# Performance work log

Measured on AMD Instinct MI355X. Metric: run time of the kernel, lower is better.

## Reference

```python
import jax, jax.numpy as jnp
import numpy as np

B, S, D = 4, 512, 256
VOCAB, MAX_RULES = 50257, 1024
EPS = 1e-12  # F.normalize default eps


def setup_inputs() -> dict:
    key = jax.random.key(0)
    k1, k2, k3, k4 = jax.random.split(key, 4)
    hidden_states = jax.random.normal(k1, (B, S, D), dtype=jnp.float32)
    token_ids = jax.random.randint(k2, (B, S), 0, VOCAB, dtype=jnp.int64)
    rule_transform = jax.random.normal(k3, (MAX_RULES, D, D), dtype=jnp.float32)
    token_rules = jax.random.randint(k4, (VOCAB,), 0, MAX_RULES, dtype=jnp.int64)
    return {
        "hidden_states": hidden_states,
        "token_ids": token_ids,
        "rule_transform": rule_transform,
        "token_rules": token_rules,
    }


def reference(hidden_states, token_ids, rule_transform, token_rules):
    # per-token rule index: [B, S]
    rule_indices = token_rules[token_ids]
    # gather DxD rule matrix per token: [B, S, D, D]
    rule_matrices = rule_transform[rule_indices]
    # F.normalize(p=2, dim=(-2,-1)): divide by Frobenius norm per matrix
    fro = jnp.sqrt(jnp.sum(rule_matrices * rule_matrices, axis=(-2, -1), keepdims=True))
    rule_matrices = rule_matrices / jnp.maximum(fro, EPS)
    # batched matvec: [B,S,D] x [B,S,D,E] -> [B,S,E]
    return jnp.einsum("bsd,bsde->bse", hidden_states, rule_matrices)
```

## Files before the change

### kernel.cpp

```cpp
#include <hip/hip_runtime.h>
#include <math.h>

#define D 256
#define NRULES 1024
#define TPB 4
#define NTOK_MAX 4096

__global__ __launch_bounds__(1024) void prep_kernel(
    const int* __restrict__ token_ids,
    const int* __restrict__ token_rules,
    int ntok,
    int* __restrict__ starts,
    int* __restrict__ bucket,
    int* __restrict__ worklist,
    int* __restrict__ nwork)
{
    __shared__ int cnt[NRULES];
    __shared__ int rtok[NTOK_MAX];
    __shared__ int wl[NRULES];
    __shared__ int nw;

    const int t = threadIdx.x;
    cnt[t] = 0;
    if (t == 0) nw = 0;
    __syncthreads();

    for (int i = t; i < ntok; i += 1024) {
        const int r = token_rules[token_ids[i]];
        rtok[i] = r;
        atomicAdd(&cnt[r], 1);
    }
    __syncthreads();

    const int c = cnt[t];

    #pragma unroll
    for (int off = 1; off < NRULES; off <<= 1) {
        const int add = (t >= off) ? cnt[t - off] : 0;
        __syncthreads();
        cnt[t] += add;
        __syncthreads();
    }
    const int incl = cnt[t];
    const int excl = incl - c;
    starts[t] = excl;
    if (t == NRULES - 1) starts[NRULES] = incl;

    if (c > TPB) wl[atomicAdd(&nw, 1)] = t;
    __syncthreads();
    if (c > 0 && c <= TPB) wl[atomicAdd(&nw, 1)] = t;

    __syncthreads();
    cnt[t] = excl;
    __syncthreads();

    for (int i = t; i < ntok; i += 1024) {
        const int pos = atomicAdd(&cnt[rtok[i]], 1);
        bucket[pos] = i;
    }

    const int nwv = nw;
    for (int i = t; i < nwv; i += 1024) worklist[i] = wl[i];
    if (t == 0) nwork[0] = nwv;
}

__global__ __launch_bounds__(256) void process_kernel(
    const float* __restrict__ hidden,
    const float* __restrict__ rules,
    const int*   __restrict__ starts,
    const int*   __restrict__ bucket,
    const int*   __restrict__ worklist,
    const int*   __restrict__ nwork,
    float* __restrict__ out)
{
    if ((int)blockIdx.x >= nwork[0]) return;
    const int r     = worklist[blockIdx.x];
    const int start = starts[r];
    const int count = starts[r + 1] - start;

    const int t    = threadIdx.x;
    const int wave = t >> 6;
    const int lane = t & 63;

    __shared__ float h_lds[TPB][D];
    __shared__ float y_lds[TPB][4][D];
    __shared__ float sq_lds[4];
    __shared__ int   toks[TPB];

    const float* __restrict__ M = rules + (size_t)r * D * D;
    const int d0  = wave << 6;
    const int col = lane << 2;

    for (int base = 0; base < count; base += TPB) {
        if (t < TPB)
            toks[t] = (base + t < count) ? bucket[start + base + t] : -1;
        #pragma unroll
        for (int j = 0; j < TPB; ++j) {
            const int idx = base + j;
            h_lds[j][t] = (idx < count)
                ? hidden[(size_t)bucket[start + idx] * D + t] : 0.f;
        }
        __syncthreads();

        float4 acc[TPB];
        #pragma unroll
        for (int j = 0; j < TPB; ++j) acc[j] = float4{0.f, 0.f, 0.f, 0.f};
        float sq = 0.f;

        #pragma unroll 4
        for (int i = 0; i < 64; ++i) {
            const int d = d0 + i;
            const float4 m = *reinterpret_cast<const float4*>(M + (size_t)d * D + col);
            sq = fmaf(m.x, m.x, fmaf(m.y, m.y, fmaf(m.z, m.z, fmaf(m.w, m.w, sq))));
            #pragma unroll
            for (int j = 0; j < TPB; ++j) {
                const float h = h_lds[j][d];
                acc[j].x = fmaf(h, m.x, acc[j].x);
                acc[j].y = fmaf(h, m.y, acc[j].y);
                acc[j].z = fmaf(h, m.z, acc[j].z);
                acc[j].w = fmaf(h, m.w, acc[j].w);
            }
        }

        #pragma unroll
        for (int off = 32; off > 0; off >>= 1)
            sq += __shfl_down(sq, off, 64);
        if (lane == 0) sq_lds[wave] = sq;

        #pragma unroll
        for (int j = 0; j < TPB; ++j)
            *reinterpret_cast<float4*>(&y_lds[j][wave][col]) = acc[j];
        __syncthreads();

        const float fro2 = sq_lds[0] + sq_lds[1] + sq_lds[2] + sq_lds[3];
        const float inv  = 1.0f / fmaxf(sqrtf(fro2), 1e-12f);

        #pragma unroll
        for (int j = 0; j < TPB; ++j) {
            const int tok = toks[j];
            if (tok >= 0) {
                const float v = (y_lds[j][0][t] + y_lds[j][1][t] +
                                 y_lds[j][2][t] + y_lds[j][3][t]) * inv;
                out[(size_t)tok * D + t] = v;
            }
        }
        __syncthreads();
    }
}

extern "C" void kernel_launch(void* const* d_in, const int* in_sizes, int n_in,
                              void* d_out, int out_size, void* d_ws, size_t ws_size,
                              hipStream_t stream) {
    const float* hidden      = (const float*)d_in[0];
    const int*   token_ids   = (const int*)d_in[1];
    const float* rules       = (const float*)d_in[2];
    const int*   token_rules = (const int*)d_in[3];
    float*       out         = (float*)d_out;

    const int ntok = in_sizes[1];

    int* ws       = (int*)d_ws;
    int* starts   = ws;
    int* bucket   = starts + NRULES + 8;
    int* worklist = bucket + ntok;
    int* nwork    = worklist + NRULES;

    prep_kernel<<<1, 1024, 0, stream>>>(
        token_ids, token_rules, ntok, starts, bucket, worklist, nwork);
    process_kernel<<<NRULES, 256, 0, stream>>>(
        hidden, rules, starts, bucket, worklist, nwork, out);
}
```

Measured before the change: 54.97 us.

## Repartition matvec work across waves, reduce with shuffles, and use wave-level scan

The per-rule matvec is re-mapped so each wave covers a 64-column slice and its lanes stride over rows. Partial sums are combined with cross-lane xor shuffles, which removes the shared-memory y buffer and lets results be stored as float4. Tokens per batch rise from 4 to 8 so each rule-matrix load is reused across more tokens, at the cost of more accumulator registers. In the prep kernel, the barrier-heavy shared-memory prefix scan is replaced by a wave-shuffle scan plus a small cross-wave scan, and one barrier is dropped.

Result: faster. 51.11 us (-7.0%).

```diff
diff --git a/kernel.cpp b/kernel.cpp
--- a/kernel.cpp
+++ b/kernel.cpp
@@ -3,7 +3,7 @@
 
 #define D 256
 #define NRULES 1024
-#define TPB 4
+#define TPB 8
 #define NTOK_MAX 4096
 
 __global__ __launch_bounds__(1024) void prep_kernel(
@@ -18,9 +18,13 @@
     __shared__ int cnt[NRULES];
     __shared__ int rtok[NTOK_MAX];
     __shared__ int wl[NRULES];
+    __shared__ int wsum[16];
     __shared__ int nw;
 
-    const int t = threadIdx.x;
+    const int t    = threadIdx.x;
+    const int wid  = t >> 6;
+    const int lane = t & 63;
+
     cnt[t] = 0;
     if (t == 0) nw = 0;
     __syncthreads();
@@ -34,24 +38,34 @@
 
     const int c = cnt[t];
 
+    int v = c;
     #pragma unroll
-    for (int off = 1; off < NRULES; off <<= 1) {
-        const int add = (t >= off) ? cnt[t - off] : 0;
-        __syncthreads();
-        cnt[t] += add;
-        __syncthreads();
+    for (int off = 1; off < 64; off <<= 1) {
+        const int u = __shfl_up(v, off, 64);
+        if (lane >= off) v += u;
     }
-    const int incl = cnt[t];
-    const int excl = incl - c;
+    if (lane == 63) wsum[wid] = v;
+    __syncthreads();
+    if (t < 16) {
+        const int w = wsum[t];
+        int s = w;
+        #pragma unroll
+        for (int off = 1; off < 16; off <<= 1) {
+            const int u = __shfl_up(s, off, 16);
+            if (t >= off) s += u;
+        }
+        wsum[t] = s - w;
+    }
+    __syncthreads();
+
+    const int excl = v - c + wsum[wid];
     starts[t] = excl;
-    if (t == NRULES - 1) starts[NRULES] = incl;
+    if (t == NRULES - 1) starts[NRULES] = excl + c;
+    cnt[t] = excl;
 
     if (c > TPB) wl[atomicAdd(&nw, 1)] = t;
     __syncthreads();
     if (c > 0 && c <= TPB) wl[atomicAdd(&nw, 1)] = t;
-
-    __syncthreads();
-    cnt[t] = excl;
     __syncthreads();
 
     for (int i = t; i < ntok; i += 1024) {
@@ -81,15 +95,14 @@
     const int t    = threadIdx.x;
     const int wave = t >> 6;
     const int lane = t & 63;
+    const int rr   = lane >> 4;
+    const int col  = (wave << 6) + ((lane & 15) << 2);
 
     __shared__ float h_lds[TPB][D];
-    __shared__ float y_lds[TPB][4][D];
     __shared__ float sq_lds[4];
     __shared__ int   toks[TPB];
 
     const float* __restrict__ M = rules + (size_t)r * D * D;
-    const int d0  = wave << 6;
-    const int col = lane << 2;
 
     for (int base = 0; base < count; base += TPB) {
         if (t < TPB)
@@ -107,9 +120,9 @@
         for (int j = 0; j < TPB; ++j) acc[j] = float4{0.f, 0.f, 0.f, 0.f};
         float sq = 0.f;
 
-        #pragma unroll 4
+        #pragma unroll 8
         for (int i = 0; i < 64; ++i) {
-            const int d = d0 + i;
+            const int d = (i << 2) + rr;
             const float4 m = *reinterpret_cast<const float4*>(M + (size_t)d * D + col);
             sq = fmaf(m.x, m.x, fmaf(m.y, m.y, fmaf(m.z, m.z, fmaf(m.w, m.w, sq))));
             #pragma unroll
@@ -128,8 +141,15 @@
         if (lane == 0) sq_lds[wave] = sq;
 
         #pragma unroll
-        for (int j = 0; j < TPB; ++j)
-            *reinterpret_cast<float4*>(&y_lds[j][wave][col]) = acc[j];
+        for (int j = 0; j < TPB; ++j) {
+            #pragma unroll
+            for (int mask = 16; mask < 64; mask <<= 1) {
+                acc[j].x += __shfl_xor(acc[j].x, mask, 64);
+                acc[j].y += __shfl_xor(acc[j].y, mask, 64);
+                acc[j].z += __shfl_xor(acc[j].z, mask, 64);
+                acc[j].w += __shfl_xor(acc[j].w, mask, 64);
+            }
+        }
         __syncthreads();
 
         const float fro2 = sq_lds[0] + sq_lds[1] + sq_lds[2] + sq_lds[3];
@@ -137,11 +157,14 @@
 
         #pragma unroll
         for (int j = 0; j < TPB; ++j) {
-            const int tok = toks[j];
-            if (tok >= 0) {
-                const float v = (y_lds[j][0][t] + y_lds[j][1][t] +
-                                 y_lds[j][2][t] + y_lds[j][3][t]) * inv;
-                out[(size_t)tok * D + t] = v;
+            if (rr == (j & 3)) {
+                const int tok = toks[j];
+                if (tok >= 0) {
+                    float4 o;
+                    o.x = acc[j].x * inv; o.y = acc[j].y * inv;
+                    o.z = acc[j].z * inv; o.w = acc[j].w * inv;
+                    *reinterpret_cast<float4*>(out + (size_t)tok * D + col) = o;
+                }
             }
         }
         __syncthreads();
```
